# Performance work log

Measured on AMD Instinct MI355X. Metric: run time of the kernel, lower is better.

## Reference

```python
import jax, jax.numpy as jnp
import numpy as np

N_USERS, N_ITEMS, DIM = 50000, 25000, 128
E_H, E_R = 600000, 1000000
N_LAYERS = 2


def setup_inputs() -> dict:
    key = jax.random.key(0)
    ks = jax.random.split(key, 20)
    nrm = lambda k, s: jax.random.normal(k, s, jnp.float32) * 0.05
    inp = {
        "u_emb": nrm(ks[0], (N_USERS, DIM)),
        "i_emb": nrm(ks[1], (N_ITEMS, DIM)),
        "gating_W": nrm(ks[2], (4, DIM, DIM)),
        "gating_b": jnp.zeros((4, DIM), jnp.float32),
        "attention": nrm(ks[3], (DIM,)),
        "attention_mat": nrm(ks[4], (DIM, DIM)),
    }
    for i, name in enumerate(["Hs", "Hj", "Hp"]):
        inp[name + "_row"] = jax.random.randint(ks[5 + 2 * i], (E_H,), 0, N_USERS, jnp.int32)
        inp[name + "_col"] = jax.random.randint(ks[6 + 2 * i], (E_H,), 0, N_USERS, jnp.int32)
        inp[name + "_val"] = jax.random.uniform(ks[11 + i], (E_H,), jnp.float32)
    inp["R_row"] = jax.random.randint(ks[14], (E_R,), 0, N_USERS, jnp.int32)
    inp["R_col"] = jax.random.randint(ks[15], (E_R,), 0, N_ITEMS, jnp.int32)
    inp["R_val"] = jnp.ones((E_R,), jnp.float32)
    return inp


def spmm(row, col, val, X, n_out):
    # sparse (n_out x n_in) @ dense (n_in x d), COO edge list form
    return jax.ops.segment_sum(val[:, None] * X[col], row, num_segments=n_out)


def l2norm(x):
    return x * jax.lax.rsqrt(jnp.maximum(jnp.sum(x * x, axis=1, keepdims=True), 1e-12))


def reference(u_emb, i_emb, gating_W, gating_b, attention, attention_mat,
              Hs_row, Hs_col, Hs_val, Hj_row, Hj_col, Hj_val,
              Hp_row, Hp_col, Hp_val, R_row, R_col, R_val):
    gate = lambda e, c: e * jax.nn.sigmoid(e @ gating_W[c] + gating_b[c])

    def chan_att(cs):
        # per-channel attention score: sum_d a_d * (E_c @ W_att)_d  -> [N, C]
        w = jnp.stack([jnp.sum(attention * (c @ attention_mat), axis=1) for c in cs], axis=1)
        s = jax.nn.softmax(w, axis=1)
        mixed = sum(s[:, k:k + 1] * cs[k] for k in range(len(cs)))
        return mixed, s

    H = [(Hs_row, Hs_col, Hs_val), (Hj_row, Hj_col, Hj_val), (Hp_row, Hp_col, Hp_val)]
    cur = [gate(u_emb, c) for c in range(3)]        # channel user embeddings
    cur_s = gate(u_emb, 3)                          # simple-gated user embeddings
    cur_i = i_emb
    all_c = [[cur[k]] for k in range(3)]
    all_i = [cur_i]
    all_s = [cur_s]
    for _ in range(N_LAYERS):
        mixed = chan_att(cur)[0] + cur_s / 2
        for k in range(3):
            r, c, v = H[k]
            cur[k] = spmm(r, c, v, cur[k], N_USERS)
            all_c[k].append(l2norm(cur[k]))
        new_item = spmm(R_col, R_row, R_val, mixed, N_ITEMS)   # R^T @ mixed
        all_i.append(l2norm(new_item))
        cur_s = spmm(R_row, R_col, R_val, cur_i, N_USERS)      # R @ item
        all_s.append(l2norm(cur_s))
        cur_i = new_item
    fc = [sum(all_c[k]) for k in range(3)]
    final_user = chan_att(fc)[0] + sum(all_s) / 2
    final_item = sum(all_i)
    return jnp.concatenate([final_user, final_item], axis=0)  # [N_USERS+N_ITEMS, DIM]
```

## Files before the change

### kernel.cpp

```cpp
#include <hip/hip_runtime.h>
#include <cstddef>
#include <cstdint>

#define NU 50000
#define NI 25000
#define DIMN 128
#define EH 600000
#define ER 1000000

typedef unsigned int u32;
typedef unsigned long long u64;
typedef __attribute__((ext_vector_type(8))) short short8;
typedef __attribute__((ext_vector_type(16))) float float16;

__device__ __forceinline__ float wave_sum64(float v) {
#pragma unroll
  for (int m = 32; m >= 1; m >>= 1) v += __shfl_xor(v, m, 64);
  return v;
}

__device__ __forceinline__ u32 pack_bf16x2(float a, float b) {
  u32 ua = __float_as_uint(a), ub = __float_as_uint(b);
  ua = (ua + 0x7fffu + ((ua >> 16) & 1u)) >> 16;
  ub = (ub + 0x7fffu + ((ub >> 16) & 1u)) >> 16;
  return ua | (ub << 16);
}
__device__ __forceinline__ u32 bf16_hi(float v) {
  u32 u = __float_as_uint(v);
  u = (u + 0x7fffu + ((u >> 16) & 1u)) & 0xffff0000u;
  return u;
}
__device__ __forceinline__ float blo(u32 p) { return __uint_as_float(p << 16); }
__device__ __forceinline__ float bhi(u32 p) { return __uint_as_float(p & 0xffff0000u); }

struct Graphs {
  const int* row[5];
  const int* col[5];
  const float* val[5];
};

__device__ __forceinline__ int g_E(int z) {
  const int E[5] = {EH, EH, EH, ER, ER};
  return E[z];
}

__global__ void k_attvec(const float* __restrict__ attm, const float* __restrict__ att,
                         float* __restrict__ attv) {
  int e = threadIdx.x;
  float s = 0.f;
  for (int d = 0; d < DIMN; ++d) s += attm[e * DIMN + d] * att[d];
  attv[e] = s;
}

__global__ void k_prepU(const float* __restrict__ U, u32* __restrict__ UP16, int n2) {
  int i = blockIdx.x * blockDim.x + threadIdx.x;
  if (i >= n2) return;
  float2 v = ((const float2*)U)[i];
  UP16[i] = pack_bf16x2(v.x, v.y);
}

__global__ void k_packW(const float* __restrict__ W, u32* __restrict__ W16) {
  int i = blockIdx.x * 256 + threadIdx.x;
  if (i >= 4 * 64 * 128) return;
  int col = i & 127, k2 = (i >> 7) & 63, c = i >> 13;
  const float* Wc = W + (size_t)c * DIMN * DIMN;
  W16[i] = pack_bf16x2(Wc[(size_t)(2 * k2) * DIMN + col], Wc[(size_t)(2 * k2 + 1) * DIMN + col]);
}

__global__ __launch_bounds__(256) void k_gate(const u32* __restrict__ UP16,
                                              const u32* __restrict__ W16,
                                              const float* __restrict__ B, u32* S16, u32* SACC,
                                              u32* G016, u32* G116, u32* G216) {
  int c = blockIdx.y;
  const u32* __restrict__ Wc = W16 + (size_t)c * (64 * 128);
  int r0 = blockIdx.x * 64;
  int t = threadIdx.x;
  int w = t >> 6, lane = t & 63;
  int ln = lane & 31, h = lane >> 5;
  int rh = w & 1, mh = w >> 1;

  __shared__ u32 ldsP[64 * 65];

  int rowl = rh * 32 + ln;
  int rg = r0 + rowl;
  int rc = (rg < NU) ? rg : (NU - 1);

  float16 acc[2];
#pragma unroll
  for (int m = 0; m < 2; ++m)
#pragma unroll
    for (int q = 0; q < 16; ++q) acc[m][q] = 0.f;

  const u32* __restrict__ urow = UP16 + (size_t)rc * 64;
#pragma unroll
  for (int kk = 0; kk < 8; ++kk) {
    int kw = kk * 8 + 4 * h;
    union {
      u32 u[4];
      short8 s;
    } bf;
#pragma unroll
    for (int j = 0; j < 4; ++j) bf.u[j] = urow[kw + j];
#pragma unroll
    for (int m = 0; m < 2; ++m) {
      union {
        u32 u[4];
        short8 s;
      } af;
      int col = 64 * mh + 32 * m + ln;
#pragma unroll
      for (int j = 0; j < 4; ++j) af.u[j] = Wc[(size_t)(kw + j) * DIMN + col];
      acc[m] = __builtin_amdgcn_mfma_f32_32x32x16_bf16(af.s, bf.s, acc[m], 0, 0, 0);
    }
  }
#pragma unroll
  for (int m = 0; m < 2; ++m)
#pragma unroll
    for (int q = 0; q < 16; q += 2) {
      int cw = 32 * mh + 16 * m + ((q & 3) >> 1) + 4 * (q >> 2) + 2 * h;
      ldsP[rowl * 65 + cw] = pack_bf16x2(acc[m][q], acc[m][q + 1]);
    }
  __syncthreads();

  int colw = t & 63, rloc = t >> 6;
  float bx = B[c * DIMN + 2 * colw], by = B[c * DIMN + 2 * colw + 1];
  u32* dst = (c == 0) ? G016 : (c == 1) ? G116 : (c == 2) ? G216 : S16;
#pragma unroll
  for (int i = 0; i < 16; ++i) {
    int row = i * 4 + rloc;
    int rg2 = r0 + row;
    if (rg2 >= NU) continue;
    u32 p = ldsP[row * 65 + colw];
    u32 uu = UP16[(size_t)rg2 * 64 + colw];
    float sx = 1.f / (1.f + __expf(-(blo(p) + bx)));
    float sy = 1.f / (1.f + __expf(-(bhi(p) + by)));
    u32 pk = pack_bf16x2(blo(uu) * sx, bhi(uu) * sy);
    dst[(size_t)rg2 * 64 + colw] = pk;
    if (c == 3) SACC[(size_t)rg2 * 64 + colw] = pk;
  }
}

__global__ void k_copy_ie(const float* __restrict__ src, float* __restrict__ dst,
                          u32* __restrict__ sh, int n2) {
  int i = blockIdx.x * blockDim.x + threadIdx.x;
  if (i >= n2) return;
  float2 v = ((const float2*)src)[i];
  ((float2*)dst)[i] = v;
  sh[i] = pack_bf16x2(v.x, v.y);
}

#define NBK 196
#define CHUNK 2048
#define FCAP 8192

__global__ __launch_bounds__(256) void k_bcount(Graphs g, int* __restrict__ bcnt) {
  int z = blockIdx.y;
  int E = g_E(z);
  if ((int)(blockIdx.x * CHUNK) >= E) return;
  int sh = (z == 4) ? 7 : 8;
  __shared__ int hist[NBK];
  for (int i = threadIdx.x; i < NBK; i += 256) hist[i] = 0;
  __syncthreads();
  const int* __restrict__ row = g.row[z];
  int e0 = blockIdx.x * CHUNK + threadIdx.x;
#pragma unroll
  for (int k = 0; k < 8; ++k) {
    int e = e0 + k * 256;
    if (e < E) atomicAdd(&hist[row[e] >> sh], 1);
  }
  __syncthreads();
  for (int i = threadIdx.x; i < NBK; i += 256)
    if (hist[i]) atomicAdd(&bcnt[z * NBK + i], hist[i]);
}

__global__ void k_bscan(const int* __restrict__ bcnt, int* __restrict__ base,
                        int* __restrict__ cur, int* __restrict__ ptr) {
  __shared__ int s[256];
  __shared__ int carry_s;
  int t = threadIdx.x;
  if (t == 0) carry_s = 0;
  __syncthreads();
  const int TOT = 5 * NBK;
  for (int c0 = 0; c0 < TOT; c0 += 256) {
    int idx = c0 + t;
    int v = (idx < TOT) ? bcnt[idx] : 0;
    s[t] = v;
    __syncthreads();
    for (int o = 1; o < 256; o <<= 1) {
      int x = (t >= o) ? s[t - o] : 0;
      __syncthreads();
      s[t] += x;
      __syncthreads();
    }
    int excl = carry_s + s[t] - v;
    if (idx < TOT) {
      base[idx] = excl;
      cur[idx] = excl;
    }
    __syncthreads();
    if (t == 0) carry_s += s[255];
    __syncthreads();
  }
  if (t == 0) base[TOT] = 3 * EH + 2 * ER;
  if (t < 5) {
    const int poffs[5] = {0, NU + 1, 2 * NU + 2, 3 * NU + 3, 4 * NU + 4};
    const int nz[5] = {NU, NU, NU, NU, NI};
    const int Ez[5] = {EH, EH, EH, ER, ER};
    ptr[poffs[t] + nz[t]] = Ez[t];
  }
}

__global__ __launch_bounds__(256) void k_bscat(Graphs g, int* __restrict__ cur,
                                               u64* __restrict__ ebkt) {
  int z = blockIdx.y;
  int E = g_E(z);
  if ((int)(blockIdx.x * CHUNK) >= E) return;
  int sh = (z == 4) ? 7 : 8;
  __shared__ int hist[NBK], basel[NBK], curl[NBK];
  for (int i = threadIdx.x; i < NBK; i += 256) {
    hist[i] = 0;
    curl[i] = 0;
  }
  __syncthreads();
  const int* __restrict__ row = g.row[z];
  const int* __restrict__ col = g.col[z];
  const float* __restrict__ val = g.val[z];
  int e0 = blockIdx.x * CHUNK + threadIdx.x;
  int r[8];
  u32 pay[8];
  bool ok[8];
#pragma unroll
  for (int k = 0; k < 8; ++k) {
    int e = e0 + k * 256;
    ok[k] = e < E;
    r[k] = ok[k] ? row[e] : 0;
    pay[k] = ok[k] ? (u32)col[e] : 0u;
  }
  if (z < 3) {
#pragma unroll
    for (int k = 0; k < 8; ++k) {
      int e = e0 + k * 256;
      if (ok[k]) pay[k] |= bf16_hi(val[e]);
    }
  }
#pragma unroll
  for (int k = 0; k < 8; ++k)
    if (ok[k]) atomicAdd(&hist[r[k] >> sh], 1);
  __syncthreads();
  for (int i = threadIdx.x; i < NBK; i += 256)
    if (hist[i]) basel[i] = atomicAdd(&cur[z * NBK + i], hist[i]);
  __syncthreads();
#pragma unroll
  for (int k = 0; k < 8; ++k)
    if (ok[k]) {
      int b = r[k] >> sh;
      int rank = atomicAdd(&curl[b], 1);
      ebkt[(size_t)(basel[b] + rank)] = ((u64)(u32)r[k] << 32) | pay[k];
    }
}

__global__ __launch_bounds__(256) void k_fine(const u64* __restrict__ ebkt,
                                              const int* __restrict__ base,
                                              u32* __restrict__ epay, int* __restrict__ ptr) {
  int z = blockIdx.y, b = blockIdx.x, t = threadIdx.x;
  int sh = (z == 4) ? 7 : 8;
  int mask = (1 << sh) - 1;
  const int poffs[5] = {0, NU + 1, 2 * NU + 2, 3 * NU + 3, 4 * NU + 4};
  const int eoffs[5] = {0, EH, 2 * EH, 3 * EH, 3 * EH + ER};
  const int nz[5] = {NU, NU, NU, NU, NI};
  int gidx = z * NBK + b;
  int s = base[gidx], e = base[gidx + 1];
  int n = e - s;
  __shared__ int cnt[256], scn[256], curl[256];
  __shared__ u32 buf[FCAP];
  cnt[t] = 0;
  curl[t] = 0;
  __syncthreads();
  for (int i = t; i < n; i += 256) {
    int row = (int)(ebkt[s + i] >> 32);
    atomicAdd(&cnt[row & mask], 1);
  }
  __syncthreads();
  int v = cnt[t];
  scn[t] = v;
  __syncthreads();
  for (int o = 1; o < 256; o <<= 1) {
    int x = (t >= o) ? scn[t - o] : 0;
    __syncthreads();
    scn[t] += x;
    __syncthreads();
  }
  int excl = scn[t] - v;
  __syncthreads();
  scn[t] = excl;
  int rg = (b << sh) + t;
  if (t <= mask && rg < nz[z]) ptr[poffs[z] + rg] = (s - eoffs[z]) + excl;
  __syncthreads();
  if (n <= FCAP) {
    for (int i = t; i < n; i += 256) {
      u64 q = ebkt[s + i];
      int r = ((int)(q >> 32)) & mask;
      int rank = atomicAdd(&curl[r], 1);
      buf[scn[r] + rank] = (u32)q;
    }
    __syncthreads();
    for (int i = t; i < n; i += 256) epay[s + i] = buf[i];
  } else {
    for (int i = t; i < n; i += 256) {
      u64 q = ebkt[s + i];
      int r = ((int)(q >> 32)) & mask;
      int rank = atomicAdd(&curl[r], 1);
      epay[s + scn[r] + rank] = (u32)q;
    }
  }
}

template <bool UNIT>
__global__ __launch_bounds__(256) void k_spmm(const int* __restrict__ ptr,
                                              const u32* __restrict__ ep,
                                              const int* __restrict__ ecol,
                                              const u32* __restrict__ X16, u32* Y16, float* ACCF,
                                              u32* ACC16, const u32* __restrict__ AINIT16,
                                              int nrows) {
  int w = blockIdx.x * 4 + __builtin_amdgcn_readfirstlane(threadIdx.x >> 6);
  int lane = threadIdx.x & 63;
  if (w >= nrows) return;
  int s = ptr[w], t = ptr[w + 1];
  float ax = 0.f, ay = 0.f;
  int e = s;
  for (; e + 8 <= t; e += 8) {
    int cc[8];
    float vv[8];
#pragma unroll
    for (int k = 0; k < 8; ++k) {
      if (UNIT) {
        cc[k] = ecol[e + k];
      } else {
        u32 q = ep[e + k];
        cc[k] = (int)(q & 0xffffu);
        vv[k] = bhi(q);
      }
    }
    u32 p[8];
#pragma unroll
    for (int k = 0; k < 8; ++k) p[k] = X16[(size_t)cc[k] * 64 + lane];
#pragma unroll
    for (int k = 0; k < 8; ++k) {
      if (UNIT) {
        ax += blo(p[k]);
        ay += bhi(p[k]);
      } else {
        ax += vv[k] * blo(p[k]);
        ay += vv[k] * bhi(p[k]);
      }
    }
  }
  for (; e + 4 <= t; e += 4) {
    int cc[4];
    float vv[4];
#pragma unroll
    for (int k = 0; k < 4; ++k) {
      if (UNIT) {
        cc[k] = ecol[e + k];
      } else {
        u32 q = ep[e + k];
        cc[k] = (int)(q & 0xffffu);
        vv[k] = bhi(q);
      }
    }
    u32 p[4];
#pragma unroll
    for (int k = 0; k < 4; ++k) p[k] = X16[(size_t)cc[k] * 64 + lane];
#pragma unroll
    for (int k = 0; k < 4; ++k) {
      if (UNIT) {
        ax += blo(p[k]);
        ay += bhi(p[k]);
      } else {
        ax += vv[k] * blo(p[k]);
        ay += vv[k] * bhi(p[k]);
      }
    }
  }
  for (; e < t; ++e) {
    int c;
    float v = 1.f;
    if (UNIT) {
      c = ecol[e];
    } else {
      u32 q = ep[e];
      c = (int)(q & 0xffffu);
      v = bhi(q);
    }
    u32 p = X16[(size_t)c * 64 + lane];
    ax += v * blo(p);
    ay += v * bhi(p);
  }
  size_t b64 = (size_t)w * 64 + lane;
  if (Y16) Y16[b64] = pack_bf16x2(ax, ay);
  if (ACCF || ACC16) {
    float ss = wave_sum64(ax * ax + ay * ay);
    float rs = rsqrtf(fmaxf(ss, 1e-12f));
    if (ACCF) {
      float2 o = *(const float2*)(ACCF + 2 * b64);
      o.x += ax * rs;
      o.y += ay * rs;
      *(float2*)(ACCF + 2 * b64) = o;
    } else {
      u32 p = AINIT16 ? AINIT16[b64] : ACC16[b64];
      float ox = blo(p) + ax * rs, oy = bhi(p) + ay * rs;
      ACC16[b64] = pack_bf16x2(ox, oy);
    }
  }
}

template <bool SRC16, bool SP16, bool OUT16>
__global__ __launch_bounds__(256) void k_mix(const void* __restrict__ c0_,
                                             const void* __restrict__ c1_,
                                             const void* __restrict__ c2_,
                                             const void* __restrict__ sp_,
                                             const float* __restrict__ attv, float* outf,
                                             u32* out16, int nrows) {
  int w = blockIdx.x * 4 + __builtin_amdgcn_readfirstlane(threadIdx.x >> 6);
  int lane = threadIdx.x & 63;
  if (w >= nrows) return;
  size_t b64 = (size_t)w * 64 + lane;
  float2 x0, x1, x2;
  if (SRC16) {
    u32 p0 = ((const u32*)c0_)[b64];
    u32 p1 = ((const u32*)c1_)[b64];
    u32 p2 = ((const u32*)c2_)[b64];
    x0 = make_float2(blo(p0), bhi(p0));
    x1 = make_float2(blo(p1), bhi(p1));
    x2 = make_float2(blo(p2), bhi(p2));
  } else {
    x0 = *(const float2*)((const float*)c0_ + 2 * b64);
    x1 = *(const float2*)((const float*)c1_ + 2 * b64);
    x2 = *(const float2*)((const float*)c2_ + 2 * b64);
  }
  float2 av = *(const float2*)(attv + lane * 2);
  float w0 = wave_sum64(x0.x * av.x + x0.y * av.y);
  float w1 = wave_sum64(x1.x * av.x + x1.y * av.y);
  float w2 = wave_sum64(x2.x * av.x + x2.y * av.y);
  float m = fmaxf(w0, fmaxf(w1, w2));
  float e0 = __expf(w0 - m), e1 = __expf(w1 - m), e2 = __expf(w2 - m);
  float inv = 1.f / (e0 + e1 + e2);
  float s0 = e0 * inv, s1 = e1 * inv, s2 = e2 * inv;
  float2 sv;
  if (SP16) {
    u32 p = ((const u32*)sp_)[b64];
    sv = make_float2(blo(p), bhi(p));
  } else {
    sv = *(const float2*)((const float*)sp_ + 2 * b64);
  }
  float ox = s0 * x0.x + s1 * x1.x + s2 * x2.x + 0.5f * sv.x;
  float oy = s0 * x0.y + s1 * x1.y + s2 * x2.y + 0.5f * sv.y;
  if (OUT16)
    out16[b64] = pack_bf16x2(ox, oy);
  else
    *(float2*)(outf + 2 * b64) = make_float2(ox, oy);
}

extern "C" void kernel_launch(void* const* d_in, const int* in_sizes, int n_in, void* d_out,
                              int out_size, void* d_ws, size_t ws_size, hipStream_t stream) {
  const float* u_emb = (const float*)d_in[0];
  const float* i_emb = (const float*)d_in[1];
  const float* gW = (const float*)d_in[2];
  const float* gB = (const float*)d_in[3];
  const float* att = (const float*)d_in[4];
  const float* attm = (const float*)d_in[5];
  Graphs g;
  g.row[0] = (const int*)d_in[6];
  g.col[0] = (const int*)d_in[7];
  g.val[0] = (const float*)d_in[8];
  g.row[1] = (const int*)d_in[9];
  g.col[1] = (const int*)d_in[10];
  g.val[1] = (const float*)d_in[11];
  g.row[2] = (const int*)d_in[12];
  g.col[2] = (const int*)d_in[13];
  g.val[2] = (const float*)d_in[14];
  g.row[3] = (const int*)d_in[15];
  g.col[3] = (const int*)d_in[16];
  g.val[3] = (const float*)d_in[17];
  g.row[4] = (const int*)d_in[16];
  g.col[4] = (const int*)d_in[15];
  g.val[4] = (const float*)d_in[17];

  const size_t U = (size_t)NU * DIMN, U64 = (size_t)NU * 64, I64 = (size_t)NI * 64;
  const size_t ETOT = 3 * (size_t)EH + 2 * (size_t)ER;
  u32* G016 = (u32*)d_ws;
  u32* G116 = G016 + U64;
  u32* G216 = G116 + U64;
  u32* C1016 = G216 + U64;
  u32* C1116 = C1016 + U64;
  u32* C1216 = C1116 + U64;
  u32* GS016 = C1216 + U64;
  u32* GS116 = GS016 + U64;
  u32* GS216 = GS116 + U64;
  u32* MIX16 = GS216 + U64;
  u32* S16 = MIX16 + U64;
  u32* SACC = S16 + U64;
  u32* I116 = SACC + U64;
  u32* IE16 = I116 + I64;
  u32* UP16 = IE16 + I64;
  u32* W16 = UP16 + U64;
  float* attv = (float*)(W16 + 32768);
  int* ptrA = (int*)(attv + DIMN);
  int* bcnt = ptrA + 225008;
  int* bbase = bcnt + 980;
  int* bcur = bbase + 984;
  uintptr_t ek_addr = ((uintptr_t)(bcur + 980) + 15u) & ~(uintptr_t)15;
  u64* ebkt = (u64*)ek_addr;
  u32* epay = (u32*)(ebkt + ETOT);
  u32* epH = epay;
  int* ecR = (int*)(epay + 3 * (size_t)EH);
  float* out_u = (float*)d_out;
  float* out_i = out_u + U;

  const int CHB = (ER + CHUNK - 1) / CHUNK;

  hipMemsetAsync(bcnt, 0, 980 * sizeof(int), stream);
  hipLaunchKernelGGL(k_bcount, dim3(CHB, 5), dim3(256), 0, stream, g, bcnt);
  hipLaunchKernelGGL(k_bscan, dim3(1), dim3(256), 0, stream, bcnt, bbase, bcur, ptrA);
  hipLaunchKernelGGL(k_bscat, dim3(CHB, 5), dim3(256), 0, stream, g, bcur, ebkt);
  hipLaunchKernelGGL(k_fine, dim3(NBK, 5), dim3(256), 0, stream, ebkt, bbase, epay, ptrA);

  hipLaunchKernelGGL(k_attvec, dim3(1), dim3(128), 0, stream, attm, att, attv);
  hipLaunchKernelGGL(k_prepU, dim3((NU * 64 + 255) / 256), dim3(256), 0, stream, u_emb, UP16,
                     NU * 64);
  hipLaunchKernelGGL(k_packW, dim3(128), dim3(256), 0, stream, gW, W16);
  hipLaunchKernelGGL(k_gate, dim3((NU + 63) / 64, 4), dim3(256), 0, stream, UP16, W16, gB, S16,
                     SACC, G016, G116, G216);
  hipLaunchKernelGGL(k_copy_ie, dim3((NI * 64 + 255) / 256), dim3(256), 0, stream, i_emb, out_i,
                     IE16, NI * 64);

  const int poffs[5] = {0, NU + 1, 2 * NU + 2, 3 * NU + 3, 4 * NU + 4};
  const int GRID_U = (NU + 3) / 4;
  const int GRID_I = (NI + 3) / 4;

  hipLaunchKernelGGL((k_mix<true, true, true>), dim3(GRID_U), dim3(256), 0, stream, G016, G116,
                     G216, S16, attv, (float*)nullptr, MIX16, NU);
  hipLaunchKernelGGL((k_spmm<true>), dim3(GRID_I), dim3(256), 0, stream, ptrA + poffs[4],
                     (const u32*)nullptr, ecR + ER, MIX16, I116, out_i, (u32*)nullptr,
                     (const u32*)nullptr, NI);
  hipLaunchKernelGGL((k_spmm<true>), dim3(GRID_U), dim3(256), 0, stream, ptrA + poffs[3],
                     (const u32*)nullptr, ecR, IE16, S16, (float*)nullptr, SACC,
                     (const u32*)nullptr, NU);
  hipLaunchKernelGGL((k_spmm<false>), dim3(GRID_U), dim3(256), 0, stream, ptrA + poffs[0], epH,
                     (const int*)nullptr, G016, C1016, (float*)nullptr, GS016, G016, NU);
  hipLaunchKernelGGL((k_spmm<false>), dim3(GRID_U), dim3(256), 0, stream, ptrA + poffs[1],
                     epH + EH, (const int*)nullptr, G116, C1116, (float*)nullptr, GS116, G116, NU);
  hipLaunchKernelGGL((k_spmm<false>), dim3(GRID_U), dim3(256), 0, stream, ptrA + poffs[2],
                     epH + 2 * (size_t)EH, (const int*)nullptr, G216, C1216, (float*)nullptr,
                     GS216, G216, NU);

  hipLaunchKernelGGL((k_mix<true, true, true>), dim3(GRID_U), dim3(256), 0, stream, C1016, C1116,
                     C1216, S16, attv, (float*)nullptr, MIX16, NU);
  hipLaunchKernelGGL((k_spmm<true>), dim3(GRID_I), dim3(256), 0, stream, ptrA + poffs[4],
                     (const u32*)nullptr, ecR + ER, MIX16, (u32*)nullptr, out_i, (u32*)nullptr,
                     (const u32*)nullptr, NI);
  hipLaunchKernelGGL((k_spmm<true>), dim3(GRID_U), dim3(256), 0, stream, ptrA + poffs[3],
                     (const u32*)nullptr, ecR, I116, (u32*)nullptr, (float*)nullptr, SACC,
                     (const u32*)nullptr, NU);
  hipLaunchKernelGGL((k_spmm<false>), dim3(GRID_U), dim3(256), 0, stream, ptrA + poffs[0], epH,
                     (const int*)nullptr, C1016, (u32*)nullptr, (float*)nullptr, GS016,
                     (const u32*)nullptr, NU);
  hipLaunchKernelGGL((k_spmm<false>), dim3(GRID_U), dim3(256), 0, stream, ptrA + poffs[1],
                     epH + EH, (const int*)nullptr, C1116, (u32*)nullptr, (float*)nullptr, GS116,
                     (const u32*)nullptr, NU);
  hipLaunchKernelGGL((k_spmm<false>), dim3(GRID_U), dim3(256), 0, stream, ptrA + poffs[2],
                     epH + 2 * (size_t)EH, (const int*)nullptr, C1216, (u32*)nullptr,
                     (float*)nullptr, GS216, (const u32*)nullptr, NU);

  hipLaunchKernelGGL((k_mix<true, true, false>), dim3(GRID_U), dim3(256), 0, stream, GS016, GS116,
                     GS216, SACC, attv, out_u, (u32*)nullptr, NU);
}
```

Measured before the change: 598.5 us.

## Batch SpMM launches, merge prep kernels, and split bucket payload/row arrays

Merges the four prep kernels (user pack, item copy, weight pack, attention vector) into one launch. Batches the independent SpMMs of each layer into multi-job launches over blockIdx.y, cutting launch count and letting small graphs share the GPU. The bucket sort now writes a 32-bit payload plus an 8-bit local row instead of a 64-bit record, and uses two half-block histograms to reduce LDS atomic contention. It also drops the duplicate SACC store from the gate kernel by initialising SACC from S16 inside the first R SpMM.

```diff
diff --git a/kernel.cpp b/kernel.cpp
--- a/kernel.cpp
+++ b/kernel.cpp
@@ -10,6 +10,7 @@
 
 typedef unsigned int u32;
 typedef unsigned long long u64;
+typedef unsigned char u8;
 typedef __attribute__((ext_vector_type(8))) short short8;
 typedef __attribute__((ext_vector_type(16))) float float16;
 
@@ -44,33 +45,42 @@
   return E[z];
 }
 
-__global__ void k_attvec(const float* __restrict__ attm, const float* __restrict__ att,
-                         float* __restrict__ attv) {
-  int e = threadIdx.x;
-  float s = 0.f;
-  for (int d = 0; d < DIMN; ++d) s += attm[e * DIMN + d] * att[d];
-  attv[e] = s;
-}
-
-__global__ void k_prepU(const float* __restrict__ U, u32* __restrict__ UP16, int n2) {
-  int i = blockIdx.x * blockDim.x + threadIdx.x;
-  if (i >= n2) return;
-  float2 v = ((const float2*)U)[i];
-  UP16[i] = pack_bf16x2(v.x, v.y);
-}
-
-__global__ void k_packW(const float* __restrict__ W, u32* __restrict__ W16) {
-  int i = blockIdx.x * 256 + threadIdx.x;
-  if (i >= 4 * 64 * 128) return;
-  int col = i & 127, k2 = (i >> 7) & 63, c = i >> 13;
-  const float* Wc = W + (size_t)c * DIMN * DIMN;
-  W16[i] = pack_bf16x2(Wc[(size_t)(2 * k2) * DIMN + col], Wc[(size_t)(2 * k2 + 1) * DIMN + col]);
+__global__ __launch_bounds__(256) void k_prep(const float* __restrict__ U, u32* __restrict__ UP16,
+                                              const float* __restrict__ IE,
+                                              float* __restrict__ out_i, u32* __restrict__ IE16,
+                                              const float* __restrict__ W, u32* __restrict__ W16,
+                                              const float* __restrict__ attm,
+                                              const float* __restrict__ att,
+                                              float* __restrict__ attv) {
+  int b = blockIdx.x;
+  if (b < 12500) {
+    int i = b * 256 + threadIdx.x;
+    float2 v = ((const float2*)U)[i];
+    UP16[i] = pack_bf16x2(v.x, v.y);
+  } else if (b < 18750) {
+    int i = (b - 12500) * 256 + threadIdx.x;
+    float2 v = ((const float2*)IE)[i];
+    ((float2*)out_i)[i] = v;
+    IE16[i] = pack_bf16x2(v.x, v.y);
+  } else if (b < 18878) {
+    int i = (b - 18750) * 256 + threadIdx.x;
+    int col = i & 127, k2 = (i >> 7) & 63, c = i >> 13;
+    const float* Wc = W + (size_t)c * DIMN * DIMN;
+    W16[i] = pack_bf16x2(Wc[(size_t)(2 * k2) * DIMN + col], Wc[(size_t)(2 * k2 + 1) * DIMN + col]);
+  } else {
+    int e = threadIdx.x;
+    if (e < 128) {
+      float s = 0.f;
+      for (int d = 0; d < DIMN; ++d) s += attm[e * DIMN + d] * att[d];
+      attv[e] = s;
+    }
+  }
 }
 
 __global__ __launch_bounds__(256) void k_gate(const u32* __restrict__ UP16,
                                               const u32* __restrict__ W16,
-                                              const float* __restrict__ B, u32* S16, u32* SACC,
-                                              u32* G016, u32* G116, u32* G216) {
+                                              const float* __restrict__ B, u32* S16, u32* G016,
+                                              u32* G116, u32* G216) {
   int c = blockIdx.y;
   const u32* __restrict__ Wc = W16 + (size_t)c * (64 * 128);
   int r0 = blockIdx.x * 64;
@@ -134,19 +144,8 @@
     u32 uu = UP16[(size_t)rg2 * 64 + colw];
     float sx = 1.f / (1.f + __expf(-(blo(p) + bx)));
     float sy = 1.f / (1.f + __expf(-(bhi(p) + by)));
-    u32 pk = pack_bf16x2(blo(uu) * sx, bhi(uu) * sy);
-    dst[(size_t)rg2 * 64 + colw] = pk;
-    if (c == 3) SACC[(size_t)rg2 * 64 + colw] = pk;
-  }
-}
-
-__global__ void k_copy_ie(const float* __restrict__ src, float* __restrict__ dst,
-                          u32* __restrict__ sh, int n2) {
-  int i = blockIdx.x * blockDim.x + threadIdx.x;
-  if (i >= n2) return;
-  float2 v = ((const float2*)src)[i];
-  ((float2*)dst)[i] = v;
-  sh[i] = pack_bf16x2(v.x, v.y);
+    dst[(size_t)rg2 * 64 + colw] = pack_bf16x2(blo(uu) * sx, bhi(uu) * sy);
+  }
 }
 
 #define NBK 196
@@ -158,19 +157,25 @@
   int E = g_E(z);
   if ((int)(blockIdx.x * CHUNK) >= E) return;
   int sh = (z == 4) ? 7 : 8;
-  __shared__ int hist[NBK];
-  for (int i = threadIdx.x; i < NBK; i += 256) hist[i] = 0;
+  __shared__ int hist[2][NBK];
+  for (int i = threadIdx.x; i < NBK; i += 256) {
+    hist[0][i] = 0;
+    hist[1][i] = 0;
+  }
   __syncthreads();
   const int* __restrict__ row = g.row[z];
   int e0 = blockIdx.x * CHUNK + threadIdx.x;
+  int half = threadIdx.x >> 7;
 #pragma unroll
   for (int k = 0; k < 8; ++k) {
     int e = e0 + k * 256;
-    if (e < E) atomicAdd(&hist[row[e] >> sh], 1);
-  }
-  __syncthreads();
-  for (int i = threadIdx.x; i < NBK; i += 256)
-    if (hist[i]) atomicAdd(&bcnt[z * NBK + i], hist[i]);
+    if (e < E) atomicAdd(&hist[half][row[e] >> sh], 1);
+  }
+  __syncthreads();
+  for (int i = threadIdx.x; i < NBK; i += 256) {
+    int tot = hist[0][i] + hist[1][i];
+    if (tot) atomicAdd(&bcnt[z * NBK + i], tot);
+  }
 }
 
 __global__ void k_bscan(const int* __restrict__ bcnt, int* __restrict__ base,
@@ -211,21 +216,25 @@
 }
 
 __global__ __launch_bounds__(256) void k_bscat(Graphs g, int* __restrict__ cur,
-                                               u64* __restrict__ ebkt) {
+                                               u32* __restrict__ epb, u8* __restrict__ erb) {
   int z = blockIdx.y;
   int E = g_E(z);
   if ((int)(blockIdx.x * CHUNK) >= E) return;
   int sh = (z == 4) ? 7 : 8;
-  __shared__ int hist[NBK], basel[NBK], curl[NBK];
+  int mask = (1 << sh) - 1;
+  __shared__ int hist[2][NBK], basel[NBK], curl[2][NBK], h0s[NBK];
   for (int i = threadIdx.x; i < NBK; i += 256) {
-    hist[i] = 0;
-    curl[i] = 0;
+    hist[0][i] = 0;
+    hist[1][i] = 0;
+    curl[0][i] = 0;
+    curl[1][i] = 0;
   }
   __syncthreads();
   const int* __restrict__ row = g.row[z];
   const int* __restrict__ col = g.col[z];
   const float* __restrict__ val = g.val[z];
   int e0 = blockIdx.x * CHUNK + threadIdx.x;
+  int half = threadIdx.x >> 7;
   int r[8];
   u32 pay[8];
   bool ok[8];
@@ -245,21 +254,28 @@
   }
 #pragma unroll
   for (int k = 0; k < 8; ++k)
-    if (ok[k]) atomicAdd(&hist[r[k] >> sh], 1);
-  __syncthreads();
-  for (int i = threadIdx.x; i < NBK; i += 256)
-    if (hist[i]) basel[i] = atomicAdd(&cur[z * NBK + i], hist[i]);
+    if (ok[k]) atomicAdd(&hist[half][r[k] >> sh], 1);
+  __syncthreads();
+  for (int i = threadIdx.x; i < NBK; i += 256) {
+    int h0 = hist[0][i];
+    int tot = h0 + hist[1][i];
+    h0s[i] = h0;
+    if (tot) basel[i] = atomicAdd(&cur[z * NBK + i], tot);
+  }
   __syncthreads();
 #pragma unroll
   for (int k = 0; k < 8; ++k)
     if (ok[k]) {
       int b = r[k] >> sh;
-      int rank = atomicAdd(&curl[b], 1);
-      ebkt[(size_t)(basel[b] + rank)] = ((u64)(u32)r[k] << 32) | pay[k];
-    }
-}
-
-__global__ __launch_bounds__(256) void k_fine(const u64* __restrict__ ebkt,
+      int rank = atomicAdd(&curl[half][b], 1);
+      int pos = basel[b] + (half ? h0s[b] : 0) + rank;
+      epb[pos] = pay[k];
+      erb[pos] = (u8)(r[k] & mask);
+    }
+}
+
+__global__ __launch_bounds__(256) void k_fine(const u32* __restrict__ epb,
+                                              const u8* __restrict__ erb,
                                               const int* __restrict__ base,
                                               u32* __restrict__ epay, int* __restrict__ ptr) {
   int z = blockIdx.y, b = blockIdx.x, t = threadIdx.x;
@@ -276,10 +292,7 @@
   cnt[t] = 0;
   curl[t] = 0;
   __syncthreads();
-  for (int i = t; i < n; i += 256) {
-    int row = (int)(ebkt[s + i] >> 32);
-    atomicAdd(&cnt[row & mask], 1);
-  }
+  for (int i = t; i < n; i += 256) atomicAdd(&cnt[erb[s + i]], 1);
   __syncthreads();
   int v = cnt[t];
   scn[t] = v;
@@ -298,33 +311,41 @@
   __syncthreads();
   if (n <= FCAP) {
     for (int i = t; i < n; i += 256) {
-      u64 q = ebkt[s + i];
-      int r = ((int)(q >> 32)) & mask;
+      int r = erb[s + i];
       int rank = atomicAdd(&curl[r], 1);
-      buf[scn[r] + rank] = (u32)q;
+      buf[scn[r] + rank] = epb[s + i];
     }
     __syncthreads();
     for (int i = t; i < n; i += 256) epay[s + i] = buf[i];
   } else {
     for (int i = t; i < n; i += 256) {
-      u64 q = ebkt[s + i];
-      int r = ((int)(q >> 32)) & mask;
+      int r = erb[s + i];
       int rank = atomicAdd(&curl[r], 1);
-      epay[s + scn[r] + rank] = (u32)q;
-    }
-  }
-}
+      epay[s + scn[r] + rank] = epb[s + i];
+    }
+  }
+}
+
+struct Job {
+  const int* ptr;
+  const u32* edges;
+  const u32* X16;
+  u32* Y16;
+  float* ACCF;
+  u32* ACC16;
+  const u32* AINIT16;
+  int nrows;
+};
 
 template <bool UNIT>
-__global__ __launch_bounds__(256) void k_spmm(const int* __restrict__ ptr,
-                                              const u32* __restrict__ ep,
-                                              const int* __restrict__ ecol,
-                                              const u32* __restrict__ X16, u32* Y16, float* ACCF,
-                                              u32* ACC16, const u32* __restrict__ AINIT16,
-                                              int nrows) {
+__global__ __launch_bounds__(256) void k_spmm(Job j0, Job j1, Job j2) {
+  Job jb = (blockIdx.y == 0) ? j0 : (blockIdx.y == 1) ? j1 : j2;
   int w = blockIdx.x * 4 + __builtin_amdgcn_readfirstlane(threadIdx.x >> 6);
   int lane = threadIdx.x & 63;
-  if (w >= nrows) return;
+  if (w >= jb.nrows) return;
+  const int* __restrict__ ptr = jb.ptr;
+  const u32* __restrict__ ep = jb.edges;
+  const u32* __restrict__ X16 = jb.X16;
   int s = ptr[w], t = ptr[w + 1];
   float ax = 0.f, ay = 0.f;
   int e = s;
@@ -333,10 +354,10 @@
     float vv[8];
 #pragma unroll
     for (int k = 0; k < 8; ++k) {
+      u32 q = ep[e + k];
       if (UNIT) {
-        cc[k] = ecol[e + k];
+        cc[k] = (int)q;
       } else {
-        u32 q = ep[e + k];
         cc[k] = (int)(q & 0xffffu);
         vv[k] = bhi(q);
       }
@@ -360,10 +381,10 @@
     float vv[4];
 #pragma unroll
     for (int k = 0; k < 4; ++k) {
+      u32 q = ep[e + k];
       if (UNIT) {
-        cc[k] = ecol[e + k];
+        cc[k] = (int)q;
       } else {
-        u32 q = ep[e + k];
         cc[k] = (int)(q & 0xffffu);
         vv[k] = bhi(q);
       }
@@ -383,12 +404,12 @@
     }
   }
   for (; e < t; ++e) {
+    u32 q = ep[e];
     int c;
     float v = 1.f;
     if (UNIT) {
-      c = ecol[e];
+      c = (int)q;
     } else {
-      u32 q = ep[e];
       c = (int)(q & 0xffffu);
       v = bhi(q);
     }
@@ -397,47 +418,41 @@
     ay += v * bhi(p);
   }
   size_t b64 = (size_t)w * 64 + lane;
-  if (Y16) Y16[b64] = pack_bf16x2(ax, ay);
-  if (ACCF || ACC16) {
+  if (jb.ACCF) {
     float ss = wave_sum64(ax * ax + ay * ay);
     float rs = rsqrtf(fmaxf(ss, 1e-12f));
-    if (ACCF) {
-      float2 o = *(const float2*)(ACCF + 2 * b64);
-      o.x += ax * rs;
-      o.y += ay * rs;
-      *(float2*)(ACCF + 2 * b64) = o;
-    } else {
-      u32 p = AINIT16 ? AINIT16[b64] : ACC16[b64];
-      float ox = blo(p) + ax * rs, oy = bhi(p) + ay * rs;
-      ACC16[b64] = pack_bf16x2(ox, oy);
-    }
-  }
-}
-
-template <bool SRC16, bool SP16, bool OUT16>
-__global__ __launch_bounds__(256) void k_mix(const void* __restrict__ c0_,
-                                             const void* __restrict__ c1_,
-                                             const void* __restrict__ c2_,
-                                             const void* __restrict__ sp_,
+    if (jb.Y16) jb.Y16[b64] = pack_bf16x2(ax, ay);
+    float2 o = *(const float2*)(jb.ACCF + 2 * b64);
+    o.x += ax * rs;
+    o.y += ay * rs;
+    *(float2*)(jb.ACCF + 2 * b64) = o;
+  } else if (jb.ACC16) {
+    float ss = wave_sum64(ax * ax + ay * ay);
+    float rs = rsqrtf(fmaxf(ss, 1e-12f));
+    u32 p = jb.AINIT16 ? jb.AINIT16[b64] : jb.ACC16[b64];
+    float ox = blo(p) + ax * rs, oy = bhi(p) + ay * rs;
+    if (jb.Y16) jb.Y16[b64] = pack_bf16x2(ax, ay);
+    jb.ACC16[b64] = pack_bf16x2(ox, oy);
+  } else if (jb.Y16) {
+    jb.Y16[b64] = pack_bf16x2(ax, ay);
+  }
+}
+
+template <bool OUT16>
+__global__ __launch_bounds__(256) void k_mix(const u32* __restrict__ c0_,
+                                             const u32* __restrict__ c1_,
+                                             const u32* __restrict__ c2_,
+                                             const u32* __restrict__ sp_,
                                              const float* __restrict__ attv, float* outf,
                                              u32* out16, int nrows) {
   int w = blockIdx.x * 4 + __builtin_amdgcn_readfirstlane(threadIdx.x >> 6);
   int lane = threadIdx.x & 63;
   if (w >= nrows) return;
   size_t b64 = (size_t)w * 64 + lane;
-  float2 x0, x1, x2;
-  if (SRC16) {
-    u32 p0 = ((const u32*)c0_)[b64];
-    u32 p1 = ((const u32*)c1_)[b64];
-    u32 p2 = ((const u32*)c2_)[b64];
-    x0 = make_float2(blo(p0), bhi(p0));
-    x1 = make_float2(blo(p1), bhi(p1));
-    x2 = make_float2(blo(p2), bhi(p2));
-  } else {
-    x0 = *(const float2*)((const float*)c0_ + 2 * b64);
-    x1 = *(const float2*)((const float*)c1_ + 2 * b64);
-    x2 = *(const float2*)((const float*)c2_ + 2 * b64);
-  }
+  u32 p0 = c0_[b64], p1 = c1_[b64], p2 = c2_[b64];
+  float2 x0 = make_float2(blo(p0), bhi(p0));
+  float2 x1 = make_float2(blo(p1), bhi(p1));
+  float2 x2 = make_float2(blo(p2), bhi(p2));
   float2 av = *(const float2*)(attv + lane * 2);
   float w0 = wave_sum64(x0.x * av.x + x0.y * av.y);
   float w1 = wave_sum64(x1.x * av.x + x1.y * av.y);
@@ -446,15 +461,9 @@
   float e0 = __expf(w0 - m), e1 = __expf(w1 - m), e2 = __expf(w2 - m);
   float inv = 1.f / (e0 + e1 + e2);
   float s0 = e0 * inv, s1 = e1 * inv, s2 = e2 * inv;
-  float2 sv;
-  if (SP16) {
-    u32 p = ((const u32*)sp_)[b64];
-    sv = make_float2(blo(p), bhi(p));
-  } else {
-    sv = *(const float2*)((const float*)sp_ + 2 * b64);
-  }
-  float ox = s0 * x0.x + s1 * x1.x + s2 * x2.x + 0.5f * sv.x;
-  float oy = s0 * x0.y + s1 * x1.y + s2 * x2.y + 0.5f * sv.y;
+  u32 ps = sp_[b64];
+  float ox = s0 * x0.x + s1 * x1.x + s2 * x2.x + 0.5f * blo(ps);
+  float oy = s0 * x0.y + s1 * x1.y + s2 * x2.y + 0.5f * bhi(ps);
   if (OUT16)
     out16[b64] = pack_bf16x2(ox, oy);
   else
@@ -509,69 +518,62 @@
   int* bcnt = ptrA + 225008;
   int* bbase = bcnt + 980;
   int* bcur = bbase + 984;
-  uintptr_t ek_addr = ((uintptr_t)(bcur + 980) + 15u) & ~(uintptr_t)15;
-  u64* ebkt = (u64*)ek_addr;
-  u32* epay = (u32*)(ebkt + ETOT);
+  uintptr_t a0 = ((uintptr_t)(bcur + 980) + 15u) & ~(uintptr_t)15;
+  u32* epb = (u32*)a0;
+  u8* erb = (u8*)(epb + ETOT);
+  uintptr_t a1 = ((uintptr_t)(erb + ETOT) + 15u) & ~(uintptr_t)15;
+  u32* epay = (u32*)a1;
   u32* epH = epay;
-  int* ecR = (int*)(epay + 3 * (size_t)EH);
+  u32* ecR = epay + 3 * (size_t)EH;
   float* out_u = (float*)d_out;
   float* out_i = out_u + U;
 
   const int CHB = (ER + CHUNK - 1) / CHUNK;
+  const int poffs[5] = {0, NU + 1, 2 * NU + 2, 3 * NU + 3, 4 * NU + 4};
+  const int GRID_U = (NU + 3) / 4;
+  const int GRID_I = (NI + 3) / 4;
 
   hipMemsetAsync(bcnt, 0, 980 * sizeof(int), stream);
   hipLaunchKernelGGL(k_bcount, dim3(CHB, 5), dim3(256), 0, stream, g, bcnt);
   hipLaunchKernelGGL(k_bscan, dim3(1), dim3(256), 0, stream, bcnt, bbase, bcur, ptrA);
-  hipLaunchKernelGGL(k_bscat, dim3(CHB, 5), dim3(256), 0, stream, g, bcur, ebkt);
-  hipLaunchKernelGGL(k_fine, dim3(NBK, 5), dim3(256), 0, stream, ebkt, bbase, epay, ptrA);
-
-  hipLaunchKernelGGL(k_attvec, dim3(1), dim3(128), 0, stream, attm, att, attv);
-  hipLaunchKernelGGL(k_prepU, dim3((NU * 64 + 255) / 256), dim3(256), 0, stream, u_emb, UP16,
-                     NU * 64);
-  hipLaunchKernelGGL(k_packW, dim3(128), dim3(256), 0, stream, gW, W16);
+  hipLaunchKernelGGL(k_bscat, dim3(CHB, 5), dim3(256), 0, stream, g, bcur, epb, erb);
+  hipLaunchKernelGGL(k_fine, dim3(NBK, 5), dim3(256), 0, stream, epb, erb, bbase, epay, ptrA);
+
+  hipLaunchKernelGGL(k_prep, dim3(18879), dim3(256), 0, stream, u_emb, UP16, i_emb, out_i, IE16,
+                     gW, W16, attm, att, attv);
   hipLaunchKernelGGL(k_gate, dim3((NU + 63) / 64, 4), dim3(256), 0, stream, UP16, W16, gB, S16,
-                     SACC, G016, G116, G216);
-  hipLaunchKernelGGL(k_copy_ie, dim3((NI * 64 + 255) / 256), dim3(256), 0, stream, i_emb, out_i,
-                     IE16, NI * 64);
-
-  const int poffs[5] = {0, NU + 1, 2 * NU + 2, 3 * NU + 3, 4 * NU + 4};
-  const int GRID_U = (NU + 3) / 4;
-  const int GRID_I = (NI + 3) / 4;
-
-  hipLaunchKernelGGL((k_mix<true, true, true>), dim3(GRID_U), dim3(256), 0, stream, G016, G116,
-                     G216, S16, attv, (float*)nullptr, MIX16, NU);
-  hipLaunchKernelGGL((k_spmm<true>), dim3(GRID_I), dim3(256), 0, stream, ptrA + poffs[4],
-                     (const u32*)nullptr, ecR + ER, MIX16, I116, out_i, (u32*)nullptr,
-                     (const u32*)nullptr, NI);
-  hipLaunchKernelGGL((k_spmm<true>), dim3(GRID_U), dim3(256), 0, stream, ptrA + poffs[3],
-                     (const u32*)nullptr, ecR, IE16, S16, (float*)nullptr, SACC,
-                     (const u32*)nullptr, NU);
-  hipLaunchKernelGGL((k_spmm<false>), dim3(GRID_U), dim3(256), 0, stream, ptrA + poffs[0], epH,
-                     (const int*)nullptr, G016, C1016, (float*)nullptr, GS016, G016, NU);
-  hipLaunchKernelGGL((k_spmm<false>), dim3(GRID_U), dim3(256), 0, stream, ptrA + poffs[1],
-                     epH + EH, (const int*)nullptr, G116, C1116, (float*)nullptr, GS116, G116, NU);
-  hipLaunchKernelGGL((k_spmm<false>), dim3(GRID_U), dim3(256), 0, stream, ptrA + poffs[2],
-                     epH + 2 * (size_t)EH, (const int*)nullptr, G216, C1216, (float*)nullptr,
-                     GS216, G216, NU);
-
-  hipLaunchKernelGGL((k_mix<true, true, true>), dim3(GRID_U), dim3(256), 0, stream, C1016, C1116,
-                     C1216, S16, attv, (float*)nullptr, MIX16, NU);
-  hipLaunchKernelGGL((k_spmm<true>), dim3(GRID_I), dim3(256), 0, stream, ptrA + poffs[4],
-                     (const u32*)nullptr, ecR + ER, MIX16, (u32*)nullptr, out_i, (u32*)nullptr,
-                     (const u32*)nullptr, NI);
-  hipLaunchKernelGGL((k_spmm<true>), dim3(GRID_U), dim3(256), 0, stream, ptrA + poffs[3],
-                     (const u32*)nullptr, ecR, I116, (u32*)nullptr, (float*)nullptr, SACC,
-                     (const u32*)nullptr, NU);
-  hipLaunchKernelGGL((k_spmm<false>), dim3(GRID_U), dim3(256), 0, stream, ptrA + poffs[0], epH,
-                     (const int*)nullptr, C1016, (u32*)nullptr, (float*)nullptr, GS016,
-                     (const u32*)nullptr, NU);
-  hipLaunchKernelGGL((k_spmm<false>), dim3(GRID_U), dim3(256), 0, stream, ptrA + poffs[1],
-                     epH + EH, (const int*)nullptr, C1116, (u32*)nullptr, (float*)nullptr, GS116,
-                     (const u32*)nullptr, NU);
-  hipLaunchKernelGGL((k_spmm<false>), dim3(GRID_U), dim3(256), 0, stream, ptrA + poffs[2],
-                     epH + 2 * (size_t)EH, (const int*)nullptr, C1216, (u32*)nullptr,
-                     (float*)nullptr, GS216, (const u32*)nullptr, NU);
-
-  hipLaunchKernelGGL((k_mix<true, true, false>), dim3(GRID_U), dim3(256), 0, stream, GS016, GS116,
-                     GS216, SACC, attv, out_u, (u32*)nullptr, NU);
-}
+                     G016, G116, G216);
+
+  Job none = {};
+
+  hipLaunchKernelGGL((k_mix<true>), dim3(GRID_U), dim3(256), 0, stream, G016, G116, G216, S16,
+                     attv, (float*)nullptr, MIX16, NU);
+  {
+    Job j0 = {ptrA + poffs[4], ecR + ER, MIX16, I116, out_i, nullptr, nullptr, NI};
+    Job j1 = {ptrA + poffs[3], ecR, IE16, S16, nullptr, SACC, S16, NU};
+    hipLaunchKernelGGL((k_spmm<true>), dim3(GRID_U, 2), dim3(256), 0, stream, j0, j1, none);
+  }
+  {
+    Job j0 = {ptrA + poffs[0], epH, G016, C1016, nullptr, GS016, G016, NU};
+    Job j1 = {ptrA + poffs[1], epH + EH, G116, C1116, nullptr, GS116, G116, NU};
+    Job j2 = {ptrA + poffs[2], epH + 2 * (size_t)EH, G216, C1216, nullptr, GS216, G216, NU};
+    hipLaunchKernelGGL((k_spmm<false>), dim3(GRID_U, 3), dim3(256), 0, stream, j0, j1, j2);
+  }
+
+  hipLaunchKernelGGL((k_mix<true>), dim3(GRID_U), dim3(256), 0, stream, C1016, C1116, C1216, S16,
+                     attv, (float*)nullptr, MIX16, NU);
+  {
+    Job j0 = {ptrA + poffs[4], ecR + ER, MIX16, nullptr, out_i, nullptr, nullptr, NI};
+    Job j1 = {ptrA + poffs[3], ecR, I116, nullptr, nullptr, SACC, nullptr, NU};
+    hipLaunchKernelGGL((k_spmm<true>), dim3(GRID_U, 2), dim3(256), 0, stream, j0, j1, none);
+  }
+  {
+    Job j0 = {ptrA + poffs[0], epH, C1016, nullptr, nullptr, GS016, nullptr, NU};
+    Job j1 = {ptrA + poffs[1], epH + EH, C1116, nullptr, nullptr, GS116, nullptr, NU};
+    Job j2 = {ptrA + poffs[2], epH + 2 * (size_t)EH, C1216, nullptr, nullptr, GS216, nullptr, NU};
+    hipLaunchKernelGGL((k_spmm<false>), dim3(GRID_U, 3), dim3(256), 0, stream, j0, j1, j2);
+  }
+
+  hipLaunchKernelGGL((k_mix<false>), dim3(GRID_U), dim3(256), 0, stream, GS016, GS116, GS216,
+                     SACC, attv, out_u, (u32*)nullptr, NU);
+}
```

Result: faster. 570.4 us (-4.7%).
